# Kernel tuning notes

Measured on AMD Instinct MI355X. Metric: run time of the kernel, lower is better.

## Reference

```python
import jax, jax.numpy as jnp
import numpy as np
import math

B, T, HID, H = 2, 2048, 2048, 16
D = HID // H  # 128
START_RATIO, RECENT_RATIO = 0.1, 0.25
ROPE_THETA = 10000.0


def setup_inputs() -> dict:
    key = jax.random.key(0)
    k1, k2, k3, k4, k5 = jax.random.split(key, 5)
    hidden_states = jax.random.normal(k1, (B, T, HID), jnp.float32)
    causal = jnp.tril(jnp.ones((T, T), bool))
    attention_mask = jnp.broadcast_to(
        jnp.where(causal, 0.0, jnp.finfo(jnp.float32).min)[None, None], (B, 1, T, T)
    )
    q_w = 0.02 * jax.random.normal(k2, (HID, HID), jnp.float32)
    k_w = 0.02 * jax.random.normal(k3, (HID, HID), jnp.float32)
    v_w = 0.02 * jax.random.normal(k4, (HID, HID), jnp.float32)
    o_w = 0.02 * jax.random.normal(k5, (HID, HID), jnp.float32)
    return dict(hidden_states=hidden_states, attention_mask=attention_mask,
                q_w=q_w, k_w=k_w, v_w=v_w, o_w=o_w)


def _rotate_half(x):
    x1, x2 = x[..., : D // 2], x[..., D // 2:]
    return jnp.concatenate([-x2, x1], axis=-1)


def _local_cam_mask(V, A_bar, recent_budget):
    # V: [B,H,K,D], A_bar: [B,H,K]
    K = V.shape[-2]
    m = recent_budget
    if m <= 0 or m >= K:
        return V
    evict_idx = max(0, min(K - m - 1, K - 1))
    ws = max(0, K - m)
    avg_window = jnp.clip(jnp.mean(A_bar[..., ws:], axis=-1), 1e-6, None)  # [B,H]
    prob = jnp.clip(A_bar[..., evict_idx] / avg_window, 0.0, 1.0)
    prob = jnp.nan_to_num(prob, nan=0.0, posinf=1.0, neginf=0.0)
    mask = jax.lax.stop_gradient(
        jax.random.bernoulli(jax.random.key(42), prob).astype(V.dtype)
    )  # [B,H]
    v_e = V[..., evict_idx, :] * mask[..., None] / m  # [B,H,D]
    return V.at[..., ws:, :].add(v_e[..., None, :])


def reference(hidden_states, attention_mask, q_w, k_w, v_w, o_w):
    MIN = jnp.finfo(hidden_states.dtype).min
    hs = jnp.nan_to_num(hidden_states, nan=0.0, posinf=1e4, neginf=-1e4)

    def proj(w):
        return (hs @ w.T).reshape(B, T, H, D).transpose(0, 2, 1, 3)  # [B,H,T,D]

    Q, K, V = proj(q_w), proj(k_w), proj(v_w)

    # rotary embedding (standard Llama)
    pos = jnp.arange(T, dtype=jnp.float32)
    inv_freq = 1.0 / (ROPE_THETA ** (jnp.arange(0, D, 2, dtype=jnp.float32) / D))
    freqs = pos[:, None] * inv_freq[None, :]  # [T, D/2]
    emb = jnp.concatenate([freqs, freqs], axis=-1)  # [T, D]
    cos, sin = jnp.cos(emb)[None, None], jnp.sin(emb)[None, None]
    Q = Q * cos + _rotate_half(Q) * sin
    K = K * cos + _rotate_half(K) * sin

    scores = jnp.einsum('bhtd,bhkd->bhtk', Q, K) / math.sqrt(D) + attention_mask
    scores = jnp.nan_to_num(scores, nan=MIN, posinf=MIN, neginf=MIN)
    attn = jax.nn.softmax(scores, axis=-1)  # [B,H,T,T]

    # first call: A_bar = detached last-row attention
    A_bar = jax.lax.stop_gradient(attn[..., -1, :])  # [B,H,T]

    k_len = T
    sb = max(0, min(int(START_RATIO * k_len), k_len))
    rb = max(0, min(int(RECENT_RATIO * k_len), k_len - sb))
    V = _local_cam_mask(V, A_bar, rb)

    attn_out = jnp.einsum('bhtk,bhkd->bhtd', attn, V)
    out = attn_out.transpose(0, 2, 1, 3).reshape(B, T, HID)
    return out @ o_w.T
```

## Files before the change

kernel.cpp:

```cpp
#include <hip/hip_runtime.h>
#include <cstdint>
#include <cstddef>


#define DEVINL __device__ __forceinline__

typedef float  f32x4  __attribute__((ext_vector_type(4)));
typedef __bf16 bf16x8 __attribute__((ext_vector_type(8)));

DEVINL float bf2f(unsigned short u){
  unsigned int x = ((unsigned int)u) << 16;
  return __builtin_bit_cast(float, x);
}
DEVINL unsigned short f2bf(float f){
  unsigned int u = __builtin_bit_cast(unsigned int, f);
  u = (u + 0x7fffu + ((u >> 16) & 1u)) >> 16;
  return (unsigned short)u;
}

DEVINL void load_lds16(const void* g, void* l){
  __builtin_amdgcn_global_load_lds(
      (const __attribute__((address_space(1))) void*)g,
      (__attribute__((address_space(3))) void*)l, 16, 0, 0);
}

#define QSCALE 0.127517432f

__global__ void cvt_all_kernel(const float* __restrict__ hs, const float* __restrict__ qw,
                               const float* __restrict__ kw, const float* __restrict__ vw,
                               const float* __restrict__ ow,
                               unsigned short* __restrict__ hsb, unsigned short* __restrict__ qwb,
                               unsigned short* __restrict__ kwb, unsigned short* __restrict__ vwb,
                               unsigned short* __restrict__ owb){
  int i = blockIdx.x * 256 + threadIdx.x;
  const float* s; unsigned short* d; int off;
  if (i < 2097152){ s = hs; d = hsb; off = i; }
  else {
    int j = i - 2097152; int w = j >> 20; off = j & 1048575;
    s = (w == 0) ? qw : (w == 1) ? kw : (w == 2) ? vw : ow;
    d = (w == 0) ? qwb : (w == 1) ? kwb : (w == 2) ? vwb : owb;
  }
  float4 v = reinterpret_cast<const float4*>(s)[off];
  uint2 o;
  o.x = (unsigned)f2bf(v.x) | ((unsigned)f2bf(v.y) << 16);
  o.y = (unsigned)f2bf(v.z) | ((unsigned)f2bf(v.w) << 16);
  reinterpret_cast<uint2*>(d)[off] = o;
}

template<int MODE>
__global__ __launch_bounds__(256, 2)
void gemm_bt_kernel(const unsigned short* __restrict__ A,
                    const unsigned short* __restrict__ B,
                    void* __restrict__ out, int M, int N, int K){
  __shared__ unsigned short As[128 * 64];
  __shared__ unsigned short Bs[128 * 64];
  const int tid = threadIdx.x, wave = tid >> 6, lane = tid & 63;
  const int m16 = lane & 15, quad = lane >> 4;
  const int m0 = blockIdx.y * 128, n0 = blockIdx.x * 128;
  const int wm = wave >> 1, wn = wave & 1;

  f32x4 acc[4][4] = {};

  for (int k0 = 0; k0 < K; k0 += 64){
    __syncthreads();
    #pragma unroll
    for (int i = 0; i < 4; ++i){
      int r  = wave * 32 + i * 8 + (lane >> 3);
      int c8 = (lane & 7) ^ (r & 7);
      load_lds16(A + (size_t)(m0 + r) * K + k0 + c8 * 8, &As[(wave * 32 + i * 8) * 64]);
      load_lds16(B + (size_t)(n0 + r) * K + k0 + c8 * 8, &Bs[(wave * 32 + i * 8) * 64]);
    }
    __syncthreads();
    #pragma unroll
    for (int kc = 0; kc < 2; ++kc){
      bf16x8 af[4], bfr[4];
      #pragma unroll
      for (int mt = 0; mt < 4; ++mt){
        int r = wm * 64 + mt * 16 + m16;
        af[mt] = *reinterpret_cast<const bf16x8*>(&As[(r * 8 + ((quad + 4 * kc) ^ (r & 7))) * 8]);
      }
      #pragma unroll
      for (int nt = 0; nt < 4; ++nt){
        int r = wn * 64 + nt * 16 + m16;
        bfr[nt] = *reinterpret_cast<const bf16x8*>(&Bs[(r * 8 + ((quad + 4 * kc) ^ (r & 7))) * 8]);
      }
      #pragma unroll
      for (int mt = 0; mt < 4; ++mt)
        #pragma unroll
        for (int nt = 0; nt < 4; ++nt)
          acc[mt][nt] = __builtin_amdgcn_mfma_f32_16x16x32_bf16(af[mt], bfr[nt], acc[mt][nt], 0, 0, 0);
    }
  }

  #pragma unroll
  for (int mt = 0; mt < 4; ++mt){
    #pragma unroll
    for (int nt = 0; nt < 4; ++nt){
      #pragma unroll
      for (int reg = 0; reg < 4; ++reg){
        int m = m0 + wm * 64 + mt * 16 + quad * 4 + reg;
        int n = n0 + wn * 64 + nt * 16 + m16;
        float v = acc[mt][nt][reg];
        if constexpr (MODE == 0){
          ((unsigned short*)out)[((((size_t)(m >> 11)) * 16 + (n >> 7)) * 2048 + (m & 2047)) * 128 + (n & 127)] = f2bf(v);
        } else if constexpr (MODE == 1){
          ((unsigned short*)out)[((((size_t)(m >> 11)) * 16 + (n >> 7)) * 128 + (n & 127)) * 2048 + (m & 2047)] = f2bf(v);
        } else {
          ((float*)out)[(size_t)m * N + n] = v;
        }
      }
    }
  }
}

__global__ void rope_kernel(unsigned short* __restrict__ Q, unsigned short* __restrict__ K){
  int gid = blockIdx.x * 256 + threadIdx.x;
  int d2 = gid & 63;
  int t  = (gid >> 6) & 2047;
  int bh = (gid >> 17) & 31;
  int isK = gid >> 22;
  unsigned short* P = isK ? K : Q;
  float sc = isK ? 1.0f : QSCALE;
  size_t base = ((size_t)bh * 2048 + t) * 128;
  float x1 = bf2f(P[base + d2]);
  float x2 = bf2f(P[base + d2 + 64]);
  float inv = expf(-(float)d2 * 0.14391156606007266f);
  float fr = (float)t * inv;
  float sn, cs;
  sincosf(fr, &sn, &cs);
  P[base + d2]      = f2bf((x1 * cs - x2 * sn) * sc);
  P[base + d2 + 64] = f2bf((x2 * cs + x1 * sn) * sc);
}

DEVINL unsigned int rotl32(unsigned int x, int r){ return (x << r) | (x >> (32 - r)); }

__device__ float threefry_u01(int i){
  unsigned int c0 = (i < 16) ? (unsigned)i : (unsigned)(i - 16);
  unsigned int c1 = (i < 16) ? (unsigned)(i + 16) : (unsigned)i;
  bool hi = (i >= 16);
  unsigned int k0 = 0u, k1 = 42u, k2 = 0x1BD11BDAu ^ k0 ^ k1;
  unsigned int ks[3] = {k0, k1, k2};
  unsigned int x0 = c0 + k0, x1 = c1 + k1;
  const int R0[4] = {13, 15, 26, 6}, R1[4] = {17, 29, 16, 24};
  #pragma unroll
  for (int r = 0; r < 5; ++r){
    const int* RR = (r & 1) ? R1 : R0;
    #pragma unroll
    for (int j = 0; j < 4; ++j){ x0 += x1; x1 = rotl32(x1, RR[j]); x1 ^= x0; }
    x0 += ks[(r + 1) % 3];
    x1 += ks[(r + 2) % 3] + (unsigned)(r + 1);
  }
  unsigned int bits = hi ? x1 : x0;
  return __builtin_bit_cast(float, (bits >> 9) | 0x3f800000u) - 1.0f;
}

DEVINL float wred_max(float v){
  #pragma unroll
  for (int m = 1; m < 64; m <<= 1) v = fmaxf(v, __shfl_xor(v, m));
  return v;
}
DEVINL float wred_sum(float v){
  #pragma unroll
  for (int m = 1; m < 64; m <<= 1) v += __shfl_xor(v, m);
  return v;
}

__global__ __launch_bounds__(256)
void cam_kernel(const unsigned short* __restrict__ Q,
                const unsigned short* __restrict__ K,
                unsigned short* __restrict__ Vt){
  const int bh = blockIdx.x, tid = threadIdx.x;
  __shared__ float qv[128];
  __shared__ float redm[4], reds[4], redw[4];
  __shared__ float e1535s;
  __shared__ float bc0;
  if (tid < 128) qv[tid] = bf2f(Q[((size_t)bh * 2048 + 2047) * 128 + tid]);
  __syncthreads();

  float sc[8];
  float smax = -1e30f;
  #pragma unroll
  for (int j = 0; j < 8; ++j){
    int k = tid + j * 256;
    const uint4* kr4 = reinterpret_cast<const uint4*>(K + ((size_t)bh * 2048 + k) * 128);
    float acc = 0.f;
    #pragma unroll
    for (int c = 0; c < 16; ++c){
      uint4 pk = kr4[c];
      acc += qv[c * 8 + 0] * bf2f((unsigned short)(pk.x & 0xffff));
      acc += qv[c * 8 + 1] * bf2f((unsigned short)(pk.x >> 16));
      acc += qv[c * 8 + 2] * bf2f((unsigned short)(pk.y & 0xffff));
      acc += qv[c * 8 + 3] * bf2f((unsigned short)(pk.y >> 16));
      acc += qv[c * 8 + 4] * bf2f((unsigned short)(pk.z & 0xffff));
      acc += qv[c * 8 + 5] * bf2f((unsigned short)(pk.z >> 16));
      acc += qv[c * 8 + 6] * bf2f((unsigned short)(pk.w & 0xffff));
      acc += qv[c * 8 + 7] * bf2f((unsigned short)(pk.w >> 16));
    }
    sc[j] = acc;
    smax = fmaxf(smax, sc[j]);
  }
  int wave = tid >> 6, lane = tid & 63;
  float wm = wred_max(smax);
  if (lane == 0) redm[wave] = wm;
  __syncthreads();
  float M = fmaxf(fmaxf(redm[0], redm[1]), fmaxf(redm[2], redm[3]));
  float tsum = 0.f, wsum = 0.f;
  #pragma unroll
  for (int j = 0; j < 8; ++j){
    int k = tid + j * 256;
    float e = exp2f(sc[j] - M);
    if (k == 1535) e1535s = e;
    tsum += e;
    if (k >= 1536) wsum += e;
  }
  tsum = wred_sum(tsum); wsum = wred_sum(wsum);
  if (lane == 0){ reds[wave] = tsum; redw[wave] = wsum; }
  __syncthreads();
  if (tid == 0){
    float sum = reds[0] + reds[1] + reds[2] + reds[3];
    float wsm = redw[0] + redw[1] + redw[2] + redw[3];
    float abar = e1535s / sum;
    float avg  = fmaxf(wsm / (512.f * sum), 1e-6f);
    float pr   = abar / avg;
    pr = fminf(fmaxf(pr, 0.f), 1.f);
    float u = threefry_u01(bh);
    bc0 = (u < pr) ? (1.f / 512.f) : 0.f;
  }
  __syncthreads();
  float ves = bc0;
  if (ves != 0.f){
    for (int idx = tid; idx < 128 * 64; idx += 256){
      int d = idx >> 6, c = idx & 63;
      unsigned short* row = Vt + ((size_t)bh * 128 + d) * 2048;
      float ve = bf2f(row[1535]) * ves;
      uint4* p = reinterpret_cast<uint4*>(row + 1536) + c;
      uint4 pk = *p;
      unsigned short h0 = f2bf(bf2f((unsigned short)(pk.x & 0xffff)) + ve);
      unsigned short h1 = f2bf(bf2f((unsigned short)(pk.x >> 16)) + ve);
      unsigned short h2 = f2bf(bf2f((unsigned short)(pk.y & 0xffff)) + ve);
      unsigned short h3 = f2bf(bf2f((unsigned short)(pk.y >> 16)) + ve);
      unsigned short h4 = f2bf(bf2f((unsigned short)(pk.z & 0xffff)) + ve);
      unsigned short h5 = f2bf(bf2f((unsigned short)(pk.z >> 16)) + ve);
      unsigned short h6 = f2bf(bf2f((unsigned short)(pk.w & 0xffff)) + ve);
      unsigned short h7 = f2bf(bf2f((unsigned short)(pk.w >> 16)) + ve);
      pk.x = (unsigned)h0 | ((unsigned)h1 << 16);
      pk.y = (unsigned)h2 | ((unsigned)h3 << 16);
      pk.z = (unsigned)h4 | ((unsigned)h5 << 16);
      pk.w = (unsigned)h6 | ((unsigned)h7 << 16);
      *p = pk;
    }
  }
}

__global__ __launch_bounds__(256, 2)
void flash_kernel(const unsigned short* __restrict__ Q,
                  const unsigned short* __restrict__ K,
                  const unsigned short* __restrict__ Vt,
                  unsigned short* __restrict__ AO){
  __shared__ unsigned short Qs[64 * 128];
  __shared__ unsigned short Ks[2][64 * 128];
  __shared__ unsigned short Vs[2][128 * 64];
  const int g = blockIdx.x, bh = blockIdx.y;
  const int tid = threadIdx.x, wave = tid >> 6, lane = tid & 63;
  const int m16 = lane & 15, quad = lane >> 4;
  unsigned short* Pw = Qs + wave * 2048;
  const int b = bh >> 4, h = bh & 15;

  #pragma unroll 1
  for (int phase = 0; phase < 2; ++phase){
    const int qt = phase ? (31 - g) : g;
    const int nk = qt + 1;

    {
      size_t qb = ((size_t)bh * 2048 + (size_t)qt * 64) * 128;
      #pragma unroll
      for (int i = 0; i < 4; ++i){
        int r   = wave * 16 + i * 4 + (lane >> 4);
        int c16 = (lane & 15) ^ (r & 15);
        load_lds16(Q + qb + (size_t)r * 128 + c16 * 8, &Qs[(wave * 16 + i * 4) * 128]);
      }
    }
    __syncthreads();
    bf16x8 qf[4];
    {
      int r = wave * 16 + m16;
      #pragma unroll
      for (int kc = 0; kc < 4; ++kc)
        qf[kc] = *reinterpret_cast<const bf16x8*>(&Qs[(r * 16 + ((quad + 4 * kc) ^ (r & 15))) * 8]);
    }

    f32x4 oacc[8] = {};
    f32x4 mst = {-1e30f, -1e30f, -1e30f, -1e30f};
    f32x4 lst = {};

    auto stageKV = [&](int kt, int buf){
      size_t kb = ((size_t)bh * 2048 + (size_t)kt * 64) * 128;
      #pragma unroll
      for (int i = 0; i < 4; ++i){
        int r   = wave * 16 + i * 4 + (lane >> 4);
        int c16 = (lane & 15) ^ (r & 15);
        load_lds16(K + kb + (size_t)r * 128 + c16 * 8, &Ks[buf][(wave * 16 + i * 4) * 128]);
      }
      size_t vb = (size_t)bh * 128 * 2048 + (size_t)kt * 64;
      #pragma unroll
      for (int i = 0; i < 4; ++i){
        int r  = wave * 32 + i * 8 + (lane >> 3);
        int c8 = (lane & 7) ^ (r & 7);
        load_lds16(Vt + vb + (size_t)r * 2048 + c8 * 8, &Vs[buf][(wave * 32 + i * 8) * 64]);
      }
    };

    stageKV(0, 0);
    #pragma unroll 1
    for (int t = 0; t < nk; ++t){
      const int buf = t & 1;
      __syncthreads();
      if (t + 1 < nk) stageKV(t + 1, buf ^ 1);

      f32x4 s[4] = {};
      #pragma unroll
      for (int kc = 0; kc < 4; ++kc){
        #pragma unroll
        for (int nt = 0; nt < 4; ++nt){
          int r = nt * 16 + m16;
          bf16x8 kf = *reinterpret_cast<const bf16x8*>(&Ks[buf][(r * 16 + ((quad + 4 * kc) ^ (r & 15))) * 8]);
          s[nt] = __builtin_amdgcn_mfma_f32_16x16x32_bf16(qf[kc], kf, s[nt], 0, 0, 0);
        }
      }
      if (t == nk - 1){
        int lrow = wave * 16 + quad * 4;
        #pragma unroll
        for (int nt = 0; nt < 4; ++nt)
          #pragma unroll
          for (int reg = 0; reg < 4; ++reg)
            if (nt * 16 + m16 > lrow + reg) s[nt][reg] = -1e30f;
      }
      #pragma unroll
      for (int reg = 0; reg < 4; ++reg){
        float rm = fmaxf(fmaxf(s[0][reg], s[1][reg]), fmaxf(s[2][reg], s[3][reg]));
        rm = fmaxf(rm, __shfl_xor(rm, 1));
        rm = fmaxf(rm, __shfl_xor(rm, 2));
        rm = fmaxf(rm, __shfl_xor(rm, 4));
        rm = fmaxf(rm, __shfl_xor(rm, 8));
        float mold = mst[reg];
        float mnew = fmaxf(mold, rm);
        float alpha = exp2f(mold - mnew);
        float rs = 0.f;
        #pragma unroll
        for (int nt = 0; nt < 4; ++nt){
          float p = exp2f(s[nt][reg] - mnew);
          s[nt][reg] = p;
          rs += p;
        }
        rs += __shfl_xor(rs, 1);
        rs += __shfl_xor(rs, 2);
        rs += __shfl_xor(rs, 4);
        rs += __shfl_xor(rs, 8);
        lst[reg] = lst[reg] * alpha + rs;
        mst[reg] = mnew;
        #pragma unroll
        for (int dt = 0; dt < 8; ++dt) oacc[dt][reg] *= alpha;
      }
      #pragma unroll
      for (int nt = 0; nt < 4; ++nt)
        #pragma unroll
        for (int reg = 0; reg < 4; ++reg){
          int r   = quad * 4 + reg;
          int col = nt * 16 + m16;
          Pw[(r * 8 + ((col >> 3) ^ (r & 7))) * 8 + (col & 7)] = f2bf(s[nt][reg]);
        }
      #pragma unroll
      for (int kc = 0; kc < 2; ++kc){
        bf16x8 pf = *reinterpret_cast<const bf16x8*>(&Pw[(m16 * 8 + ((quad + 4 * kc) ^ (m16 & 7))) * 8]);
        #pragma unroll
        for (int dt = 0; dt < 8; ++dt){
          int r = dt * 16 + m16;
          bf16x8 vf = *reinterpret_cast<const bf16x8*>(&Vs[buf][(r * 8 + ((quad + 4 * kc) ^ (r & 7))) * 8]);
          oacc[dt] = __builtin_amdgcn_mfma_f32_16x16x32_bf16(pf, vf, oacc[dt], 0, 0, 0);
        }
      }
    }

    #pragma unroll
    for (int reg = 0; reg < 4; ++reg){
      int tq = qt * 64 + wave * 16 + quad * 4 + reg;
      float inv = 1.0f / lst[reg];
      size_t ob = ((size_t)b * 2048 + tq) * 2048 + (size_t)h * 128;
      #pragma unroll
      for (int dt = 0; dt < 8; ++dt)
        AO[ob + dt * 16 + m16] = f2bf(oacc[dt][reg] * inv);
    }
  }
}

extern "C" void kernel_launch(void* const* d_in, const int* in_sizes, int n_in,
                              void* d_out, int out_size, void* d_ws, size_t ws_size,
                              hipStream_t stream){
  const float* hs = (const float*)d_in[0];
  const float* qw = (const float*)d_in[2];
  const float* kw = (const float*)d_in[3];
  const float* vw = (const float*)d_in[4];
  const float* ow = (const float*)d_in[5];

  char* ws = (char*)d_ws;
  const size_t MB = 1ull << 20;
  unsigned short* hsb = (unsigned short*)(ws);
  unsigned short* qwb = (unsigned short*)(ws + 16 * MB);
  unsigned short* kwb = (unsigned short*)(ws + 24 * MB);
  unsigned short* vwb = (unsigned short*)(ws + 32 * MB);
  unsigned short* owb = (unsigned short*)(ws + 40 * MB);
  unsigned short* Qb  = (unsigned short*)(ws + 48 * MB);
  unsigned short* Kb  = (unsigned short*)(ws + 64 * MB);
  unsigned short* Vtb = (unsigned short*)(ws + 80 * MB);
  unsigned short* AOb = (unsigned short*)(ws + 96 * MB);

  cvt_all_kernel<<<24576, 256, 0, stream>>>(hs, qw, kw, vw, ow, hsb, qwb, kwb, vwb, owb);

  dim3 g(16, 32);
  gemm_bt_kernel<0><<<g, 256, 0, stream>>>(hsb, qwb, Qb,  4096, 2048, 2048);
  gemm_bt_kernel<0><<<g, 256, 0, stream>>>(hsb, kwb, Kb,  4096, 2048, 2048);
  gemm_bt_kernel<1><<<g, 256, 0, stream>>>(hsb, vwb, Vtb, 4096, 2048, 2048);

  rope_kernel<<<32768, 256, 0, stream>>>(Qb, Kb);
  cam_kernel<<<32, 256, 0, stream>>>(Qb, Kb, Vtb);
  flash_kernel<<<dim3(16, 32), 256, 0, stream>>>(Qb, Kb, Vtb, AOb);

  gemm_bt_kernel<2><<<g, 256, 0, stream>>>(AOb, owb, d_out, 4096, 2048, 2048);
}
```

Measured before the change: 461.2 us.

## Fuse QKV projections into one GEMM and compute softmax row sums via MFMA

The three Q/K/V projection GEMMs become one launch over a 6144-wide N dimension. This works because the bf16 Q, K and V weights sit next to each other in the workspace, and the epilogue routes each column range to the Q, K or transposed V layout. The flash kernel stops doing shuffle-based row-sum reductions: it accumulates the softmax denominator with an extra MFMA against a ones vector and rescales accumulators as whole vectors. The manual bf16 rounding is replaced by the native __bf16 conversion, and the GEMM launch bounds rise to three blocks per CU, which may cause register spills.

```diff
diff --git a/kernel.cpp b/kernel.cpp
--- a/kernel.cpp
+++ b/kernel.cpp
@@ -12,10 +12,8 @@
   unsigned int x = ((unsigned int)u) << 16;
   return __builtin_bit_cast(float, x);
 }
-DEVINL unsigned short f2bf(float f){
-  unsigned int u = __builtin_bit_cast(unsigned int, f);
-  u = (u + 0x7fffu + ((u >> 16) & 1u)) >> 16;
-  return (unsigned short)u;
+DEVINL void store_bf(unsigned short* p, float f){
+  *(__bf16*)p = (__bf16)f;
 }
 
 DEVINL void load_lds16(const void* g, void* l){
@@ -41,17 +39,18 @@
     d = (w == 0) ? qwb : (w == 1) ? kwb : (w == 2) ? vwb : owb;
   }
   float4 v = reinterpret_cast<const float4*>(s)[off];
-  uint2 o;
-  o.x = (unsigned)f2bf(v.x) | ((unsigned)f2bf(v.y) << 16);
-  o.y = (unsigned)f2bf(v.z) | ((unsigned)f2bf(v.w) << 16);
-  reinterpret_cast<uint2*>(d)[off] = o;
+  unsigned short o[4];
+  store_bf(&o[0], v.x); store_bf(&o[1], v.y); store_bf(&o[2], v.z); store_bf(&o[3], v.w);
+  reinterpret_cast<uint2*>(d)[off] = *reinterpret_cast<uint2*>(o);
 }
 
 template<int MODE>
-__global__ __launch_bounds__(256, 2)
+__global__ __launch_bounds__(256, 3)
 void gemm_bt_kernel(const unsigned short* __restrict__ A,
                     const unsigned short* __restrict__ B,
-                    void* __restrict__ out, int M, int N, int K){
+                    unsigned short* __restrict__ Qo, unsigned short* __restrict__ Ko,
+                    unsigned short* __restrict__ Vo, float* __restrict__ Co,
+                    int M, int N, int K){
   __shared__ unsigned short As[128 * 64];
   __shared__ unsigned short Bs[128 * 64];
   const int tid = threadIdx.x, wave = tid >> 6, lane = tid & 63;
@@ -102,11 +101,17 @@
         int n = n0 + wn * 64 + nt * 16 + m16;
         float v = acc[mt][nt][reg];
         if constexpr (MODE == 0){
-          ((unsigned short*)out)[((((size_t)(m >> 11)) * 16 + (n >> 7)) * 2048 + (m & 2047)) * 128 + (n & 127)] = f2bf(v);
-        } else if constexpr (MODE == 1){
-          ((unsigned short*)out)[((((size_t)(m >> 11)) * 16 + (n >> 7)) * 128 + (n & 127)) * 2048 + (m & 2047)] = f2bf(v);
+          int which = n >> 11;
+          int nn = n & 2047;
+          int bq = m >> 11, t = m & 2047, hd = nn >> 7, dd = nn & 127;
+          if (which == 0)
+            store_bf(&Qo[((((size_t)bq) * 16 + hd) * 2048 + t) * 128 + dd], v);
+          else if (which == 1)
+            store_bf(&Ko[((((size_t)bq) * 16 + hd) * 2048 + t) * 128 + dd], v);
+          else
+            store_bf(&Vo[((((size_t)bq) * 16 + hd) * 128 + dd) * 2048 + t], v);
         } else {
-          ((float*)out)[(size_t)m * N + n] = v;
+          Co[(size_t)m * N + n] = v;
         }
       }
     }
@@ -128,8 +133,8 @@
   float fr = (float)t * inv;
   float sn, cs;
   sincosf(fr, &sn, &cs);
-  P[base + d2]      = f2bf((x1 * cs - x2 * sn) * sc);
-  P[base + d2 + 64] = f2bf((x2 * cs + x1 * sn) * sc);
+  store_bf(&P[base + d2],      (x1 * cs - x2 * sn) * sc);
+  store_bf(&P[base + d2 + 64], (x2 * cs + x1 * sn) * sc);
 }
 
 DEVINL unsigned int rotl32(unsigned int x, int r){ return (x << r) | (x >> (32 - r)); }
@@ -235,18 +240,19 @@
       float ve = bf2f(row[1535]) * ves;
       uint4* p = reinterpret_cast<uint4*>(row + 1536) + c;
       uint4 pk = *p;
-      unsigned short h0 = f2bf(bf2f((unsigned short)(pk.x & 0xffff)) + ve);
-      unsigned short h1 = f2bf(bf2f((unsigned short)(pk.x >> 16)) + ve);
-      unsigned short h2 = f2bf(bf2f((unsigned short)(pk.y & 0xffff)) + ve);
-      unsigned short h3 = f2bf(bf2f((unsigned short)(pk.y >> 16)) + ve);
-      unsigned short h4 = f2bf(bf2f((unsigned short)(pk.z & 0xffff)) + ve);
-      unsigned short h5 = f2bf(bf2f((unsigned short)(pk.z >> 16)) + ve);
-      unsigned short h6 = f2bf(bf2f((unsigned short)(pk.w & 0xffff)) + ve);
-      unsigned short h7 = f2bf(bf2f((unsigned short)(pk.w >> 16)) + ve);
-      pk.x = (unsigned)h0 | ((unsigned)h1 << 16);
-      pk.y = (unsigned)h2 | ((unsigned)h3 << 16);
-      pk.z = (unsigned)h4 | ((unsigned)h5 << 16);
-      pk.w = (unsigned)h6 | ((unsigned)h7 << 16);
+      unsigned short h[8];
+      store_bf(&h[0], bf2f((unsigned short)(pk.x & 0xffff)) + ve);
+      store_bf(&h[1], bf2f((unsigned short)(pk.x >> 16)) + ve);
+      store_bf(&h[2], bf2f((unsigned short)(pk.y & 0xffff)) + ve);
+      store_bf(&h[3], bf2f((unsigned short)(pk.y >> 16)) + ve);
+      store_bf(&h[4], bf2f((unsigned short)(pk.z & 0xffff)) + ve);
+      store_bf(&h[5], bf2f((unsigned short)(pk.z >> 16)) + ve);
+      store_bf(&h[6], bf2f((unsigned short)(pk.w & 0xffff)) + ve);
+      store_bf(&h[7], bf2f((unsigned short)(pk.w >> 16)) + ve);
+      pk.x = (unsigned)h[0] | ((unsigned)h[1] << 16);
+      pk.y = (unsigned)h[2] | ((unsigned)h[3] << 16);
+      pk.z = (unsigned)h[4] | ((unsigned)h[5] << 16);
+      pk.w = (unsigned)h[6] | ((unsigned)h[7] << 16);
       *p = pk;
     }
   }
@@ -266,6 +272,10 @@
   unsigned short* Pw = Qs + wave * 2048;
   const int b = bh >> 4, h = bh & 15;
 
+  bf16x8 onesf;
+  #pragma unroll
+  for (int j = 0; j < 8; ++j) onesf[j] = (__bf16)1.0f;
+
   #pragma unroll 1
   for (int phase = 0; phase < 2; ++phase){
     const int qt = phase ? (31 - g) : g;
@@ -290,8 +300,8 @@
     }
 
     f32x4 oacc[8] = {};
+    f32x4 oaccL = {};
     f32x4 mst = {-1e30f, -1e30f, -1e30f, -1e30f};
-    f32x4 lst = {};
 
     auto stageKV = [&](int kt, int buf){
       size_t kb = ((size_t)bh * 2048 + (size_t)kt * 64) * 128;
@@ -335,6 +345,7 @@
           for (int reg = 0; reg < 4; ++reg)
             if (nt * 16 + m16 > lrow + reg) s[nt][reg] = -1e30f;
       }
+      f32x4 av;
       #pragma unroll
       for (int reg = 0; reg < 4; ++reg){
         float rm = fmaxf(fmaxf(s[0][reg], s[1][reg]), fmaxf(s[2][reg], s[3][reg]));
@@ -344,34 +355,28 @@
         rm = fmaxf(rm, __shfl_xor(rm, 8));
         float mold = mst[reg];
         float mnew = fmaxf(mold, rm);
-        float alpha = exp2f(mold - mnew);
-        float rs = 0.f;
-        #pragma unroll
-        for (int nt = 0; nt < 4; ++nt){
-          float p = exp2f(s[nt][reg] - mnew);
-          s[nt][reg] = p;
-          rs += p;
-        }
-        rs += __shfl_xor(rs, 1);
-        rs += __shfl_xor(rs, 2);
-        rs += __shfl_xor(rs, 4);
-        rs += __shfl_xor(rs, 8);
-        lst[reg] = lst[reg] * alpha + rs;
+        av[reg] = exp2f(mold - mnew);
         mst[reg] = mnew;
         #pragma unroll
-        for (int dt = 0; dt < 8; ++dt) oacc[dt][reg] *= alpha;
-      }
+        for (int nt = 0; nt < 4; ++nt)
+          s[nt][reg] = exp2f(s[nt][reg] - mnew);
+      }
+      oaccL *= av;
+      #pragma unroll
+      for (int dt = 0; dt < 8; ++dt) oacc[dt] *= av;
+
       #pragma unroll
       for (int nt = 0; nt < 4; ++nt)
         #pragma unroll
         for (int reg = 0; reg < 4; ++reg){
           int r   = quad * 4 + reg;
           int col = nt * 16 + m16;
-          Pw[(r * 8 + ((col >> 3) ^ (r & 7))) * 8 + (col & 7)] = f2bf(s[nt][reg]);
+          store_bf(&Pw[(r * 8 + ((col >> 3) ^ (r & 7))) * 8 + (col & 7)], s[nt][reg]);
         }
       #pragma unroll
       for (int kc = 0; kc < 2; ++kc){
         bf16x8 pf = *reinterpret_cast<const bf16x8*>(&Pw[(m16 * 8 + ((quad + 4 * kc) ^ (m16 & 7))) * 8]);
+        oaccL = __builtin_amdgcn_mfma_f32_16x16x32_bf16(pf, onesf, oaccL, 0, 0, 0);
         #pragma unroll
         for (int dt = 0; dt < 8; ++dt){
           int r = dt * 16 + m16;
@@ -384,11 +389,11 @@
     #pragma unroll
     for (int reg = 0; reg < 4; ++reg){
       int tq = qt * 64 + wave * 16 + quad * 4 + reg;
-      float inv = 1.0f / lst[reg];
+      float inv = 1.0f / oaccL[reg];
       size_t ob = ((size_t)b * 2048 + tq) * 2048 + (size_t)h * 128;
       #pragma unroll
       for (int dt = 0; dt < 8; ++dt)
-        AO[ob + dt * 16 + m16] = f2bf(oacc[dt][reg] * inv);
+        store_bf(&AO[ob + dt * 16 + m16], oacc[dt][reg] * inv);
     }
   }
 }
@@ -416,14 +421,13 @@
 
   cvt_all_kernel<<<24576, 256, 0, stream>>>(hs, qw, kw, vw, ow, hsb, qwb, kwb, vwb, owb);
 
-  dim3 g(16, 32);
-  gemm_bt_kernel<0><<<g, 256, 0, stream>>>(hsb, qwb, Qb,  4096, 2048, 2048);
-  gemm_bt_kernel<0><<<g, 256, 0, stream>>>(hsb, kwb, Kb,  4096, 2048, 2048);
-  gemm_bt_kernel<1><<<g, 256, 0, stream>>>(hsb, vwb, Vtb, 4096, 2048, 2048);
+  gemm_bt_kernel<0><<<dim3(48, 32), 256, 0, stream>>>(hsb, qwb, Qb, Kb, Vtb, nullptr,
+                                                      4096, 6144, 2048);
 
   rope_kernel<<<32768, 256, 0, stream>>>(Qb, Kb);
   cam_kernel<<<32, 256, 0, stream>>>(Qb, Kb, Vtb);
   flash_kernel<<<dim3(16, 32), 256, 0, stream>>>(Qb, Kb, Vtb, AOb);
 
-  gemm_bt_kernel<2><<<g, 256, 0, stream>>>(AOb, owb, d_out, 4096, 2048, 2048);
-}
+  gemm_bt_kernel<2><<<dim3(16, 32), 256, 0, stream>>>(AOb, owb, nullptr, nullptr, nullptr,
+                                                      (float*)d_out, 4096, 2048, 2048);
+}
```

After: 458.8 us. About the same (-0.5%).
